# Kernel tuning notes

Hardware: AMD Instinct MI355X
Metric: run time of the kernel (lower is better)

The kernel has to match this reference:

```python
import jax, jax.numpy as jnp
import numpy as np
import math

N_LAYERS = 2; D = 768; D_INNER = 1536; N = 16; DR = 48; K = 4
VOCAB = 32000; B = 2; L = 1024
EPS = 1e-5


def setup_inputs() -> dict:
    key = jax.random.key(0)
    k = jax.random.split(key, 10)
    x = jax.random.randint(k[0], (B, L), 0, VOCAB)
    embedding = jax.random.normal(k[1], (VOCAB, D), jnp.float32) * 0.02
    rms_w = jnp.ones((N_LAYERS, D), jnp.float32)
    in_proj_w = jax.random.normal(k[2], (N_LAYERS, 2 * D_INNER, D), jnp.float32) * 0.02
    conv_w = jax.random.normal(k[3], (N_LAYERS, D_INNER, K), jnp.float32) * 0.1
    conv_b = jnp.zeros((N_LAYERS, D_INNER), jnp.float32)
    # S4D-real init: A[d, n] = n+1, stored as log(-A) = log(A)
    A0 = jnp.log(jnp.broadcast_to(jnp.arange(1, N + 1, dtype=jnp.float32), (D_INNER, N)))
    log_minus_A = jnp.tile(A0[None], (N_LAYERS, 1, 1))
    bcdelta_w = jax.random.normal(k[4], (N_LAYERS, 2 * N + DR, D_INNER), jnp.float32) * 0.02
    s = DR ** -0.5  # delta_init='random', delta_scale=1.0
    dup_w = jax.random.uniform(k[5], (N_LAYERS, D_INNER, DR), jnp.float32, minval=-s, maxval=s)
    u = jax.random.uniform(k[6], (N_LAYERS, D_INNER), jnp.float32)
    samp = jnp.maximum(jnp.exp((math.log(0.1) - math.log(0.001)) * u + math.log(0.001)), 1e-4)
    dup_b = samp + jnp.log(-jnp.expm1(-samp))  # softplus-inverse
    D_param = jnp.ones((N_LAYERS, D_INNER), jnp.float32)
    out_proj_w = jax.random.normal(k[7], (N_LAYERS, D, D_INNER), jnp.float32) * (0.02 / math.sqrt(N_LAYERS))
    norm_f_w = jnp.ones((D,), jnp.float32)
    return dict(x=x, embedding=embedding, rms_w=rms_w, in_proj_w=in_proj_w,
                conv_w=conv_w, conv_b=conv_b, log_minus_A=log_minus_A,
                bcdelta_w=bcdelta_w, dup_w=dup_w, dup_b=dup_b,
                D_param=D_param, out_proj_w=out_proj_w, norm_f_w=norm_f_w)


def _rmsnorm(h, w):
    return h * jax.lax.rsqrt(jnp.mean(h * h, axis=-1, keepdims=True) + EPS) * w


def _causal_conv(h, w, b):
    # depthwise causal conv: torch Conv1d(pad=K-1)[..., :L]
    hp = jnp.pad(h, ((0, 0), (K - 1, 0), (0, 0)))  # (b, l+K-1, d)
    Lh = h.shape[1]
    y = sum(hp[:, k:k + Lh, :] * w[:, k] for k in range(K))
    return y + b


def _s6(h, lA, bcw, dw, db, Dp):
    bcd = h @ bcw.T                                    # (b, l, 2N+DR)
    Bm, Cm, dlt = jnp.split(bcd, [N, 2 * N], axis=-1)
    delta = jax.nn.softplus(dlt @ dw.T + db)           # (b, l, d)
    A = -jnp.exp(lA)                                   # (d, n), negative
    dA = jnp.einsum('bld,dn->bldn', delta, A)
    A_bar = jnp.exp(dA)
    B_bar = (A_bar - 1.0) / dA * jnp.einsum('bld,bln->bldn', delta, Bm)
    u = B_bar * h[..., None]                           # (b, l, d, n)

    def step(hs, inp):
        a, ui, c = inp
        hs = a * hs + ui                               # (b, d, n)
        return hs, jnp.einsum('bn,bdn->bd', c, hs)

    h0 = jnp.zeros((h.shape[0], h.shape[2], N), h.dtype)
    _, ys = jax.lax.scan(step, h0, (jnp.swapaxes(A_bar, 0, 1),
                                    jnp.swapaxes(u, 0, 1),
                                    jnp.swapaxes(Cm, 0, 1)))
    return jnp.swapaxes(ys, 0, 1) + h * Dp


def _block(h, in_w, cw, cb, lA, bcw, dw, db, Dp, ow):
    xz = h @ in_w.T
    xi, res = jnp.split(xz, 2, axis=-1)
    xi = jax.nn.silu(_causal_conv(xi, cw, cb))
    y = _s6(xi, lA, bcw, dw, db, Dp)
    return (y * jax.nn.silu(res)) @ ow.T


def reference(x, embedding, rms_w, in_proj_w, conv_w, conv_b, log_minus_A,
              bcdelta_w, dup_w, dup_b, D_param, out_proj_w, norm_f_w):
    h = embedding[x]                                   # (b, l, D)
    for i in range(N_LAYERS):
        h = _block(_rmsnorm(h, rms_w[i]), in_proj_w[i], conv_w[i], conv_b[i],
                   log_minus_A[i], bcdelta_w[i], dup_w[i], dup_b[i],
                   D_param[i], out_proj_w[i]) + h
    h = _rmsnorm(h, norm_f_w)
    return h @ embedding.T                             # tied logits (b, l, V)
```

## Files before the change

kernel.cpp:

```cpp
#include <hip/hip_runtime.h>
#include <math.h>

#define BB 2
#define LL 1024
#define DD 768
#define DI 1536
#define NS 16
#define DRR 48
#define KC 4
#define VOC 32000
#define BT (BB*LL)
#define EPS 1e-5f

#define NCH 16
#define TC  (LL/NCH)
#define CHW ((DI/16)*256)

typedef __attribute__((ext_vector_type(4))) float f32x4;
typedef __attribute__((ext_vector_type(8))) short short8;
typedef unsigned short ushort_t;

__device__ __forceinline__ unsigned short f2bf(float f) {
    unsigned int u = __float_as_uint(f);
    u += 0x7FFFu + ((u >> 16) & 1u);
    return (unsigned short)(u >> 16);
}

#define GLDS(gp, lp) __builtin_amdgcn_global_load_lds( \
    (const __attribute__((address_space(1))) unsigned int*)(gp), \
    (__attribute__((address_space(3))) unsigned int*)(lp), 16, 0, 0)

#define DPP_ADD(c, ctrl) ((c) + __int_as_float(__builtin_amdgcn_update_dpp( \
    0, __float_as_int(c), (ctrl), 0xF, 0xF, true)))

template<bool ADD, bool NMASK, bool ATOMIC>
__global__ __launch_bounds__(256) void gemm_bf16(
    const ushort_t* __restrict__ A, const ushort_t* __restrict__ W,
    float* C, int Nn, int lda, int ldc, int kchunk)
{
    __shared__ __align__(16) ushort_t As[128 * 32];
    __shared__ __align__(16) ushort_t Ws[128 * 32];

    const int row0 = blockIdx.x * 128;
    const int col0 = blockIdx.y * 128;
    const int tid  = threadIdx.x;
    const int lane = tid & 63;
    const int wave = tid >> 6;
    const int wm   = (wave & 1) * 64;
    const int wn   = (wave >> 1) * 64;
    const int mrow = lane & 15;
    const int quad = lane >> 4;

    const int kb = blockIdx.z * kchunk;

    const int srow = tid >> 2;
    const int scol = (tid & 3) << 3;
    const ushort_t* gA0 = A + (size_t)(row0 + srow) * lda + scol;
    const ushort_t* gA1 = A + (size_t)(row0 + 64 + srow) * lda + scol;
    const ushort_t* gW0 = W + (size_t)(col0 + srow) * lda + scol;
    const ushort_t* gW1 = W + (size_t)(col0 + 64 + srow) * lda + scol;
    char* lA0 = (char*)As + wave * 1024;
    char* lA1 = (char*)As + 4096 + wave * 1024;
    char* lW0 = (char*)Ws + wave * 1024;
    char* lW1 = (char*)Ws + 4096 + wave * 1024;

    f32x4 acc[4][4];
#pragma unroll
    for (int i = 0; i < 4; ++i)
#pragma unroll
        for (int j = 0; j < 4; ++j)
            acc[i][j] = (f32x4){0.f, 0.f, 0.f, 0.f};

    for (int k0 = kb; k0 < kb + kchunk; k0 += 32) {
        GLDS(gA0 + k0, lA0);
        GLDS(gA1 + k0, lA1);
        GLDS(gW0 + k0, lW0);
        GLDS(gW1 + k0, lW1);
        __syncthreads();

        short8 af[4], wf[4];
#pragma unroll
        for (int i = 0; i < 4; ++i) {
            af[i] = *(const short8*)&As[(wm + i * 16 + mrow) * 32 + quad * 8];
            wf[i] = *(const short8*)&Ws[(wn + i * 16 + mrow) * 32 + quad * 8];
        }
#pragma unroll
        for (int i = 0; i < 4; ++i)
#pragma unroll
            for (int j = 0; j < 4; ++j)
                acc[i][j] = __builtin_amdgcn_mfma_f32_16x16x32_bf16(
                    af[i], wf[j], acc[i][j], 0, 0, 0);
        __syncthreads();
    }

#pragma unroll
    for (int i = 0; i < 4; ++i)
#pragma unroll
        for (int j = 0; j < 4; ++j)
#pragma unroll
            for (int r = 0; r < 4; ++r) {
                int row = row0 + wm + i * 16 + quad * 4 + r;
                int col = col0 + wn + j * 16 + mrow;
                if (!NMASK || col < Nn) {
                    float v = acc[i][j][r];
                    size_t off = (size_t)row * ldc + col;
                    if (ATOMIC) {
                        atomicAdd(&C[off], v);
                    } else {
                        if (ADD) v += C[off];
                        C[off] = v;
                    }
                }
            }
}

#define GK  768
#define GN  32000
#define NT12 12

__device__ __forceinline__ void stage_unit(
    int j, char* ldsw, const char* sA0, const char* sA1,
    const char* sB0, const char* sB1)
{
    if (j >= 4 * NT12) return;
    int tt = j >> 2, hh = (j >> 1) & 1, ee = j & 1;
    int koff = tt * 128 + hh * 64;
    char* dst = ldsw + (j & 7) * 16384;
    const char* s0 = (ee ? sB0 : sA0) + koff;
    const char* s1 = (ee ? sB1 : sA1) + koff;
    GLDS(s0, dst);
    GLDS(s1, dst + 8192);
}

#define VMCNT(N) asm volatile("s_waitcnt vmcnt(" #N ")" ::: "memory")

#define SBAR() do { __builtin_amdgcn_sched_barrier(0); \
    __builtin_amdgcn_s_barrier(); \
    __builtin_amdgcn_sched_barrier(0); } while (0)

#define MFMA16(M2) do { \
    __builtin_amdgcn_s_setprio(1); \
    _Pragma("unroll") \
    for (int i_ = 0; i_ < 4; ++i_) \
        _Pragma("unroll") \
        for (int n_ = 0; n_ < 4; ++n_) \
            acc[(M2)*4 + i_][n_] = __builtin_amdgcn_mfma_f32_16x16x32_bf16( \
                af[i_], wf[n_], acc[(M2)*4 + i_][n_], 0, 0, 0); \
    __builtin_amdgcn_s_setprio(0); \
} while (0)

#define PHASE(T, H, M2, LOADB, WAITSTMT) do { \
    const char* bufA_ = ldsc + ((T) & 1) * 65536 + (H) * 32768; \
    if (LOADB) { \
        _Pragma("unroll") \
        for (int n_ = 0; n_ < 4; ++n_) \
            wf[n_] = *(const short8*)(bufA_ + 16384 + offB[n_]); \
    } \
    _Pragma("unroll") \
    for (int i_ = 0; i_ < 4; ++i_) \
        af[i_] = *(const short8*)(bufA_ + offA[(M2)*4 + i_]); \
    stage_unit(4*(T) + 2*(H) + (M2) + 6, ldsw, sA0, sA1, sB0, sB1); \
    SBAR(); \
    MFMA16(M2); \
    WAITSTMT; \
    SBAR(); \
} while (0)

#define TILE(T, W1, W2) do { \
    PHASE(T, 0, 0, true,  (void)0); \
    PHASE(T, 0, 1, false, W1); \
    PHASE(T, 1, 0, true,  (void)0); \
    PHASE(T, 1, 1, false, W2); \
} while (0)

__global__ __launch_bounds__(512, 2) void gemm_logits_256(
    const ushort_t* __restrict__ A, const ushort_t* __restrict__ W,
    float* __restrict__ C)
{
    __shared__ __align__(16) char ldsc[131072];

    const int bid = blockIdx.x;
    const int s   = (bid & 7) * 125 + (bid >> 3);
    const int mt  = s & 7;
    const int nt  = s >> 3;

    const int tid  = threadIdx.x;
    const int lane = tid & 63;
    const int wave = tid >> 6;
    const int wm   = wave >> 2;
    const int wn   = wave & 3;
    const int mrow = lane & 15;
    const int quad = lane >> 4;

    int offA[8], offB[4];
#pragma unroll
    for (int m = 0; m < 8; ++m) {
        int r = wm * 128 + m * 16 + mrow;
        offA[m] = r * 64 + ((quad * 16) ^ (((r >> 1) & 3) << 4));
    }
#pragma unroll
    for (int n = 0; n < 4; ++n) {
        int r = wn * 64 + n * 16 + mrow;
        offB[n] = r * 64 + ((quad * 16) ^ (((r >> 1) & 3) << 4));
    }

    const int X0 = tid * 16;
    const int L0 = X0 ^ (((X0 >> 7) & 3) << 4);
    const int r0 = L0 >> 6, c0 = L0 & 63;
    const char* sA0 = (const char*)A + ((size_t)(mt * 256 +       r0) * GK) * 2 + c0;
    const char* sA1 = (const char*)A + ((size_t)(mt * 256 + 128 + r0) * GK) * 2 + c0;
    const char* sB0 = (const char*)W + ((size_t)(nt * 256 +       r0) * GK) * 2 + c0;
    const char* sB1 = (const char*)W + ((size_t)(nt * 256 + 128 + r0) * GK) * 2 + c0;
    char* ldsw = ldsc + wave * 1024;

    f32x4 acc[8][4];
#pragma unroll
    for (int m = 0; m < 8; ++m)
#pragma unroll
        for (int n = 0; n < 4; ++n)
            acc[m][n] = (f32x4){0.f, 0.f, 0.f, 0.f};

    short8 af[4], wf[4];

#pragma unroll
    for (int j = 0; j < 6; ++j)
        stage_unit(j, ldsw, sA0, sA1, sB0, sB1);
    VMCNT(8);
    SBAR();

    for (int t = 0; t < NT12 - 2; ++t)
        TILE(t, VMCNT(8), VMCNT(8));
    TILE(10, VMCNT(8), VMCNT(4));
    TILE(11, VMCNT(0), (void)0);

    float* Cb = C + (size_t)(mt * 256 + wm * 128 + quad * 4) * GN
                  + nt * 256 + wn * 64 + mrow;
#pragma unroll
    for (int m = 0; m < 8; ++m)
#pragma unroll
        for (int r = 0; r < 4; ++r)
#pragma unroll
            for (int n = 0; n < 4; ++n)
                Cb[(size_t)(m * 16 + r) * GN + n * 16] = acc[m][n][r];
}

__global__ __launch_bounds__(256) void cvt_bf16_kernel(
    const float* __restrict__ in, ushort_t* __restrict__ out, int n4)
{
    int i = blockIdx.x * 256 + threadIdx.x;
    if (i >= n4) return;
    float4 v = ((const float4*)in)[i];
    ushort4 o;
    o.x = f2bf(v.x); o.y = f2bf(v.y); o.z = f2bf(v.z); o.w = f2bf(v.w);
    ((ushort4*)out)[i] = o;
}

__global__ __launch_bounds__(256) void cvt_bcw_kernel(
    const float* __restrict__ bcw, ushort_t* __restrict__ out)
{
    int i = blockIdx.x * 256 + threadIdx.x;
    if (i >= 2 * 128 * 1536 / 4) return;
    int e = i * 4;
    int layer = e / (128 * 1536);
    int rem = e % (128 * 1536);
    int row = rem / 1536, col = rem % 1536;
    ushort4 o = {0, 0, 0, 0};
    if (row < 80) {
        float4 v = *(const float4*)(bcw + ((size_t)layer * 80 + row) * 1536 + col);
        o.x = f2bf(v.x); o.y = f2bf(v.y); o.z = f2bf(v.z); o.w = f2bf(v.w);
    }
    ((ushort4*)out)[i] = o;
}

__global__ __launch_bounds__(256) void zero_kernel(float* __restrict__ p, int n)
{
    int i = blockIdx.x * 256 + threadIdx.x;
    if (i < n) p[i] = 0.f;
}

__global__ __launch_bounds__(256) void embed_kernel(
    const int* __restrict__ x, const float* __restrict__ emb, float* __restrict__ h)
{
    int idx = blockIdx.x * 256 + threadIdx.x;
    if (idx >= BT * (DD / 4)) return;
    int row = idx / (DD / 4), c = idx % (DD / 4);
    ((float4*)h)[idx] = ((const float4*)(emb + (size_t)x[row] * DD))[c];
}

__global__ __launch_bounds__(256) void rmsnorm_kernel(
    const float* __restrict__ h, const float* __restrict__ w, ushort_t* __restrict__ out)
{
    int row = blockIdx.x, tid = threadIdx.x;
    const float* hr = h + (size_t)row * DD;
    float s = 0.f;
    for (int i = tid; i < DD; i += 256) { float v = hr[i]; s += v * v; }
#pragma unroll
    for (int off = 32; off >= 1; off >>= 1) s += __shfl_xor(s, off);
    __shared__ float part[4];
    if ((tid & 63) == 0) part[tid >> 6] = s;
    __syncthreads();
    float tot = part[0] + part[1] + part[2] + part[3];
    float sc = rsqrtf(tot * (1.0f / DD) + EPS);
    for (int i = tid; i < DD; i += 256)
        out[(size_t)row * DD + i] = f2bf(hr[i] * sc * w[i]);
}

__global__ __launch_bounds__(256) void conv_silu_kernel(
    const float* __restrict__ xz, const float* __restrict__ cw,
    const float* __restrict__ cb, float* __restrict__ xi, ushort_t* __restrict__ xi16)
{
    int idx = blockIdx.x * 256 + threadIdx.x;
    if (idx >= BT * DI) return;
    int d = idx % DI, bt = idx / DI, t = bt % LL;
    const float* base = xz + (size_t)bt * (2 * DI) + d;
    float w0 = cw[d * 4 + 0], w1 = cw[d * 4 + 1], w2 = cw[d * 4 + 2], w3 = cw[d * 4 + 3];
    float acc = cb[d] + base[0] * w3;
    if (t >= 1) acc += base[-(ptrdiff_t)(2 * DI)] * w2;
    if (t >= 2) acc += base[-(ptrdiff_t)(4 * DI)] * w1;
    if (t >= 3) acc += base[-(ptrdiff_t)(6 * DI)] * w0;
    float v = acc / (1.0f + expf(-acc));
    xi[idx] = v;
    xi16[idx] = f2bf(v);
}

__global__ __launch_bounds__(256) void delta_kernel(
    const float* __restrict__ bcd, const float* __restrict__ dw,
    const float* __restrict__ db, float* __restrict__ delta)
{
    int row = blockIdx.x / 6, chunk = blockIdx.x % 6;
    int d = chunk * 256 + threadIdx.x;
    __shared__ float dlt_s[DRR];
    if (threadIdx.x < DRR) dlt_s[threadIdx.x] = bcd[(size_t)row * 80 + 32 + threadIdx.x];
    __syncthreads();
    float z = db[d];
    const float* wr = dw + (size_t)d * DRR;
#pragma unroll
    for (int r = 0; r < DRR; ++r) z = fmaf(dlt_s[r], wr[r], z);
    delta[(size_t)row * DI + d] = (z > 20.f) ? z : log1pf(expf(z));
}

__global__ __launch_bounds__(256) void scan_pass1(
    const float* __restrict__ delta, const float* __restrict__ xi,
    const float* __restrict__ bcd, const float* __restrict__ lA,
    float* __restrict__ a_cum, float* __restrict__ h_end)
{
    int blk  = blockIdx.x;
    int c    = blk % NCH;
    int rest = blk / NCH;
    int b    = rest / (DI / 16);
    int dbi  = rest % (DI / 16);
    int dblk = dbi * 16;
    int tid  = threadIdx.x, lane = tid & 63, wave = tid >> 6;
    int n = lane & 15, dl = wave * 4 + (lane >> 4), d = dblk + dl;

    float Av   = -expf(lA[(size_t)d * NS + n]);
    float A2   = Av * 1.44269504088896f;
    float invA = 1.0f / Av;

    __shared__ float2 s_dx[TC][16];
    __shared__ float  s_B [TC][16];

    const float* dbase = delta + ((size_t)b * LL + c * TC) * DI + dblk;
    const float* xbase = xi    + ((size_t)b * LL + c * TC) * DI + dblk;
    const float* bcb   = bcd   + ((size_t)b * LL + c * TC) * 80;

    for (int i = tid; i < TC * 16; i += 256) {
        int tt = i >> 4, dd = i & 15;
        s_dx[tt][dd] = make_float2(dbase[(size_t)tt * DI + dd],
                                   xbase[(size_t)tt * DI + dd]);
        s_B[tt][dd]  = bcb[(size_t)tt * 80 + dd];
    }
    __syncthreads();

    float hs = 0.f, sd = 0.f;
#pragma unroll 4
    for (int tt = 0; tt < TC; ++tt) {
        float2 dx = s_dx[tt][dl];
        float Bv  = s_B[tt][n];
        float Ab  = exp2f(dx.x * A2);
        float u   = (Ab - 1.0f) * invA * Bv * dx.y;
        hs = fmaf(Ab, hs, u);
        sd += dx.x;
    }
    size_t o = (((size_t)b * NCH + c) * (DI / 16) + dbi) * 256 + dl * 16 + n;
    a_cum[o] = exp2f(A2 * sd);
    h_end[o] = hs;
}

__global__ __launch_bounds__(256) void scan_pass2(
    const float* __restrict__ a_cum, const float* __restrict__ h_end,
    float* __restrict__ h_init)
{
    int gid = blockIdx.x * 256 + threadIdx.x;
    if (gid >= BB * CHW) return;
    int b = gid / CHW, r = gid % CHW;
    size_t base = (size_t)b * NCH * CHW + r;
    float h = 0.f;
#pragma unroll
    for (int c = 0; c < NCH; ++c) {
        h_init[base + (size_t)c * CHW] = h;
        h = fmaf(a_cum[base + (size_t)c * CHW], h, h_end[base + (size_t)c * CHW]);
    }
}

__global__ __launch_bounds__(256) void scan_pass3(
    const float* __restrict__ delta, const float* __restrict__ xi,
    const float* __restrict__ bcd, const float* __restrict__ lA,
    const float* __restrict__ Dp, const float* __restrict__ h_init,
    float* __restrict__ y)
{
    int blk  = blockIdx.x;
    int c    = blk % NCH;
    int rest = blk / NCH;
    int b    = rest / (DI / 16);
    int dbi  = rest % (DI / 16);
    int dblk = dbi * 16;
    int tid  = threadIdx.x, lane = tid & 63, wave = tid >> 6;
    int n = lane & 15, dl = wave * 4 + (lane >> 4), d = dblk + dl;

    float Av   = -expf(lA[(size_t)d * NS + n]);
    float A2   = Av * 1.44269504088896f;
    float invA = 1.0f / Av;
    float Dpv  = Dp[d];

    __shared__ float2 s_dx[TC][16];
    __shared__ float2 s_bc[TC][16];

    const float* dbase = delta + ((size_t)b * LL + c * TC) * DI + dblk;
    const float* xbase = xi    + ((size_t)b * LL + c * TC) * DI + dblk;
    const float* bcb   = bcd   + ((size_t)b * LL + c * TC) * 80;
    float*       ybase = y     + ((size_t)b * LL + c * TC) * DI + dblk;

    for (int i = tid; i < TC * 16; i += 256) {
        int tt = i >> 4, dd = i & 15;
        s_dx[tt][dd] = make_float2(dbase[(size_t)tt * DI + dd],
                                   xbase[(size_t)tt * DI + dd]);
        s_bc[tt][dd] = make_float2(bcb[(size_t)tt * 80 + dd],
                                   bcb[(size_t)tt * 80 + 16 + dd]);
    }
    __syncthreads();

    float hs = h_init[(((size_t)b * NCH + c) * (DI / 16) + dbi) * 256 + dl * 16 + n];

#pragma unroll 4
    for (int tt = 0; tt < TC; ++tt) {
        float2 dx = s_dx[tt][dl];
        float2 bc = s_bc[tt][n];
        float Ab  = exp2f(dx.x * A2);
        float u   = (Ab - 1.0f) * invA * bc.x * dx.y;
        hs = fmaf(Ab, hs, u);
        float r = bc.y * hs;
        r = DPP_ADD(r, 0xB1);
        r = DPP_ADD(r, 0x4E);
        r = DPP_ADD(r, 0x141);
        r = DPP_ADD(r, 0x140);
        if (n == 0) ybase[(size_t)tt * DI + dl] = fmaf(dx.y, Dpv, r);
    }
}

__global__ __launch_bounds__(256) void gate_kernel(
    const float* __restrict__ y, const float* __restrict__ xz, ushort_t* __restrict__ yg16)
{
    int idx = blockIdx.x * 256 + threadIdx.x;
    if (idx >= BT * DI) return;
    int d = idx % DI, bt = idx / DI;
    float r = xz[(size_t)bt * (2 * DI) + DI + d];
    yg16[idx] = f2bf(y[idx] * r / (1.0f + expf(-r)));
}

extern "C" void kernel_launch(void* const* d_in, const int* in_sizes, int n_in,
                              void* d_out, int out_size, void* d_ws, size_t ws_size,
                              hipStream_t stream)
{
    const int*   x    = (const int*)  d_in[0];
    const float* emb  = (const float*)d_in[1];
    const float* rmsw = (const float*)d_in[2];
    const float* inw  = (const float*)d_in[3];
    const float* cw   = (const float*)d_in[4];
    const float* cb   = (const float*)d_in[5];
    const float* lA   = (const float*)d_in[6];
    const float* bcw  = (const float*)d_in[7];
    const float* dw   = (const float*)d_in[8];
    const float* db   = (const float*)d_in[9];
    const float* Dp   = (const float*)d_in[10];
    const float* ow   = (const float*)d_in[11];
    const float* nfw  = (const float*)d_in[12];
    float* out = (float*)d_out;

    float* ws = (float*)d_ws;
    float* h    = ws;
    float* xz   = h    + (size_t)BT * DD;
    float* xi   = xz   + (size_t)BT * 2 * DI;
    float* bcd  = xi   + (size_t)BT * DI;
    float* dlt  = bcd  + (size_t)BT * 80;
    float* yb   = dlt  + (size_t)BT * DI;
    float* acum = yb   + (size_t)BT * DI;
    float* hend = acum + (size_t)BB * NCH * DI * NS;
    float* hini = hend + (size_t)BB * NCH * DI * NS;
    ushort_t* bf = (ushort_t*)(hini + (size_t)BB * NCH * DI * NS);
    ushort_t* hn_bf  = bf;
    ushort_t* xib_bf = hn_bf  + (size_t)BT * DD;
    ushort_t* yg_bf  = xib_bf + (size_t)BT * DI;
    ushort_t* emb_bf = yg_bf  + (size_t)BT * DI;
    ushort_t* inw_bf = emb_bf + (size_t)VOC * DD;
    ushort_t* ow_bf  = inw_bf + (size_t)2 * 2 * DI * DD;
    ushort_t* bcw_bf = ow_bf  + (size_t)2 * DD * DI;

    cvt_bf16_kernel<<<(VOC * DD / 4 + 255) / 256, 256, 0, stream>>>(emb, emb_bf, VOC * DD / 4);
    cvt_bf16_kernel<<<(2 * 2 * DI * DD / 4 + 255) / 256, 256, 0, stream>>>(inw, inw_bf, 2 * 2 * DI * DD / 4);
    cvt_bf16_kernel<<<(2 * DD * DI / 4 + 255) / 256, 256, 0, stream>>>(ow, ow_bf, 2 * DD * DI / 4);
    cvt_bcw_kernel<<<(2 * 128 * 1536 / 4 + 255) / 256, 256, 0, stream>>>(bcw, bcw_bf);

    embed_kernel<<<(BT * (DD / 4) + 255) / 256, 256, 0, stream>>>(x, emb, h);

    for (int layer = 0; layer < 2; ++layer) {
        rmsnorm_kernel<<<BT, 256, 0, stream>>>(h, rmsw + (size_t)layer * DD, hn_bf);

        gemm_bf16<false, false, false><<<dim3(BT / 128, 2 * DI / 128, 1), 256, 0, stream>>>(
            hn_bf, inw_bf + (size_t)layer * 2 * DI * DD, xz, 2 * DI, DD, 2 * DI, DD);

        conv_silu_kernel<<<(BT * DI + 255) / 256, 256, 0, stream>>>(
            xz, cw + (size_t)layer * DI * KC, cb + (size_t)layer * DI, xi, xib_bf);

        zero_kernel<<<(BT * 80 + 255) / 256, 256, 0, stream>>>(bcd, BT * 80);

        gemm_bf16<false, true, true><<<dim3(BT / 128, 1, 8), 256, 0, stream>>>(
            xib_bf, bcw_bf + (size_t)layer * 128 * 1536, bcd, 80, DI, 80, DI / 8);

        delta_kernel<<<BT * 6, 256, 0, stream>>>(
            bcd, dw + (size_t)layer * DI * DRR, db + (size_t)layer * DI, dlt);

        scan_pass1<<<BB * (DI / 16) * NCH, 256, 0, stream>>>(
            dlt, xi, bcd, lA + (size_t)layer * DI * NS, acum, hend);
        scan_pass2<<<(BB * CHW + 255) / 256, 256, 0, stream>>>(acum, hend, hini);
        scan_pass3<<<BB * (DI / 16) * NCH, 256, 0, stream>>>(
            dlt, xi, bcd, lA + (size_t)layer * DI * NS, Dp + (size_t)layer * DI, hini, yb);

        gate_kernel<<<(BT * DI + 255) / 256, 256, 0, stream>>>(yb, xz, yg_bf);

        gemm_bf16<true, false, false><<<dim3(BT / 128, DD / 128, 1), 256, 0, stream>>>(
            yg_bf, ow_bf + (size_t)layer * DD * DI, h, DD, DI, DD, DI);
    }

    rmsnorm_kernel<<<BT, 256, 0, stream>>>(h, nfw, hn_bf);

    gemm_logits_256<<<dim3(BT / 256 * (VOC / 256)), 512, 0, stream>>>(
        hn_bf, emb_bf, out);
}
```

Measured before the change: 880.4 us.

## Double-buffer GEMM LDS, fuse embed+norm, gate into scan, split-K out_proj

Makes the bf16 GEMM double-buffered in LDS so the next K-tile's global loads are issued while MFMAs run on the current tile. It fuses the embedding gather with the first RMSNorm, folds the bcd zeroing into the conv kernel, and moves the SiLU gate into scan_pass3 so the fp32 y buffer and the separate gate kernel go away. The out_proj GEMM becomes split-K by 4 with atomic adds into h, and the logits stores become nontemporal. These changes cut launches and intermediate memory traffic, at the cost of double the GEMM LDS use, atomic contention, and nondeterministic summation order.

```diff
diff --git a/kernel.cpp b/kernel.cpp
--- a/kernel.cpp
+++ b/kernel.cpp
@@ -38,8 +38,8 @@
     const ushort_t* __restrict__ A, const ushort_t* __restrict__ W,
     float* C, int Nn, int lda, int ldc, int kchunk)
 {
-    __shared__ __align__(16) ushort_t As[128 * 32];
-    __shared__ __align__(16) ushort_t Ws[128 * 32];
+    __shared__ __align__(16) ushort_t As[2 * 128 * 32];
+    __shared__ __align__(16) ushort_t Ws[2 * 128 * 32];
 
     const int row0 = blockIdx.x * 128;
     const int col0 = blockIdx.y * 128;
@@ -50,8 +50,7 @@
     const int wn   = (wave >> 1) * 64;
     const int mrow = lane & 15;
     const int quad = lane >> 4;
-
-    const int kb = blockIdx.z * kchunk;
+    const int kb   = blockIdx.z * kchunk;
 
     const int srow = tid >> 2;
     const int scol = (tid & 3) << 3;
@@ -59,10 +58,13 @@
     const ushort_t* gA1 = A + (size_t)(row0 + 64 + srow) * lda + scol;
     const ushort_t* gW0 = W + (size_t)(col0 + srow) * lda + scol;
     const ushort_t* gW1 = W + (size_t)(col0 + 64 + srow) * lda + scol;
-    char* lA0 = (char*)As + wave * 1024;
-    char* lA1 = (char*)As + 4096 + wave * 1024;
-    char* lW0 = (char*)Ws + wave * 1024;
-    char* lW1 = (char*)Ws + 4096 + wave * 1024;
+
+#define STAGE_MM(buf, kk) do { \
+    char* a_ = (char*)As + (buf) * 8192 + wave * 1024; \
+    char* w_ = (char*)Ws + (buf) * 8192 + wave * 1024; \
+    GLDS(gA0 + (kk), a_); GLDS(gA1 + (kk), a_ + 4096); \
+    GLDS(gW0 + (kk), w_); GLDS(gW1 + (kk), w_ + 4096); \
+} while (0)
 
     f32x4 acc[4][4];
 #pragma unroll
@@ -71,18 +73,20 @@
         for (int j = 0; j < 4; ++j)
             acc[i][j] = (f32x4){0.f, 0.f, 0.f, 0.f};
 
+    STAGE_MM(0, kb);
+    __syncthreads();
+
+    int cur = 0;
     for (int k0 = kb; k0 < kb + kchunk; k0 += 32) {
-        GLDS(gA0 + k0, lA0);
-        GLDS(gA1 + k0, lA1);
-        GLDS(gW0 + k0, lW0);
-        GLDS(gW1 + k0, lW1);
-        __syncthreads();
-
+        if (k0 + 32 < kb + kchunk) STAGE_MM(cur ^ 1, k0 + 32);
+
+        const ushort_t* Ab = As + cur * 4096;
+        const ushort_t* Wb = Ws + cur * 4096;
         short8 af[4], wf[4];
 #pragma unroll
         for (int i = 0; i < 4; ++i) {
-            af[i] = *(const short8*)&As[(wm + i * 16 + mrow) * 32 + quad * 8];
-            wf[i] = *(const short8*)&Ws[(wn + i * 16 + mrow) * 32 + quad * 8];
+            af[i] = *(const short8*)&Ab[(wm + i * 16 + mrow) * 32 + quad * 8];
+            wf[i] = *(const short8*)&Wb[(wn + i * 16 + mrow) * 32 + quad * 8];
         }
 #pragma unroll
         for (int i = 0; i < 4; ++i)
@@ -91,7 +95,9 @@
                 acc[i][j] = __builtin_amdgcn_mfma_f32_16x16x32_bf16(
                     af[i], wf[j], acc[i][j], 0, 0, 0);
         __syncthreads();
-    }
+        cur ^= 1;
+    }
+#undef STAGE_MM
 
 #pragma unroll
     for (int i = 0; i < 4; ++i)
@@ -241,7 +247,8 @@
         for (int r = 0; r < 4; ++r)
 #pragma unroll
             for (int n = 0; n < 4; ++n)
-                Cb[(size_t)(m * 16 + r) * GN + n * 16] = acc[m][n][r];
+                __builtin_nontemporal_store(acc[m][n][r],
+                    &Cb[(size_t)(m * 16 + r) * GN + n * 16]);
 }
 
 __global__ __launch_bounds__(256) void cvt_bf16_kernel(
@@ -272,19 +279,26 @@
     ((ushort4*)out)[i] = o;
 }
 
-__global__ __launch_bounds__(256) void zero_kernel(float* __restrict__ p, int n)
-{
-    int i = blockIdx.x * 256 + threadIdx.x;
-    if (i < n) p[i] = 0.f;
-}
-
-__global__ __launch_bounds__(256) void embed_kernel(
-    const int* __restrict__ x, const float* __restrict__ emb, float* __restrict__ h)
-{
-    int idx = blockIdx.x * 256 + threadIdx.x;
-    if (idx >= BT * (DD / 4)) return;
-    int row = idx / (DD / 4), c = idx % (DD / 4);
-    ((float4*)h)[idx] = ((const float4*)(emb + (size_t)x[row] * DD))[c];
+__global__ __launch_bounds__(256) void embed_norm_kernel(
+    const int* __restrict__ x, const float* __restrict__ emb,
+    const float* __restrict__ w, float* __restrict__ h, ushort_t* __restrict__ out)
+{
+    int row = blockIdx.x, tid = threadIdx.x;
+    const float* er = emb + (size_t)x[row] * DD;
+    float v0 = er[tid], v1 = er[tid + 256], v2 = er[tid + 512];
+    float s = v0 * v0 + v1 * v1 + v2 * v2;
+#pragma unroll
+    for (int off = 32; off >= 1; off >>= 1) s += __shfl_xor(s, off);
+    __shared__ float part[4];
+    if ((tid & 63) == 0) part[tid >> 6] = s;
+    __syncthreads();
+    float sc = rsqrtf((part[0] + part[1] + part[2] + part[3]) * (1.0f / DD) + EPS);
+    float* hr = h + (size_t)row * DD;
+    hr[tid] = v0; hr[tid + 256] = v1; hr[tid + 512] = v2;
+    ushort_t* o = out + (size_t)row * DD;
+    o[tid]       = f2bf(v0 * sc * w[tid]);
+    o[tid + 256] = f2bf(v1 * sc * w[tid + 256]);
+    o[tid + 512] = f2bf(v2 * sc * w[tid + 512]);
 }
 
 __global__ __launch_bounds__(256) void rmsnorm_kernel(
@@ -307,10 +321,12 @@
 
 __global__ __launch_bounds__(256) void conv_silu_kernel(
     const float* __restrict__ xz, const float* __restrict__ cw,
-    const float* __restrict__ cb, float* __restrict__ xi, ushort_t* __restrict__ xi16)
+    const float* __restrict__ cb, float* __restrict__ xi, ushort_t* __restrict__ xi16,
+    float* __restrict__ bcd)
 {
     int idx = blockIdx.x * 256 + threadIdx.x;
     if (idx >= BT * DI) return;
+    if (idx < BT * 80) bcd[idx] = 0.f;
     int d = idx % DI, bt = idx / DI, t = bt % LL;
     const float* base = xz + (size_t)bt * (2 * DI) + d;
     float w0 = cw[d * 4 + 0], w1 = cw[d * 4 + 1], w2 = cw[d * 4 + 2], w3 = cw[d * 4 + 3];
@@ -407,7 +423,7 @@
     const float* __restrict__ delta, const float* __restrict__ xi,
     const float* __restrict__ bcd, const float* __restrict__ lA,
     const float* __restrict__ Dp, const float* __restrict__ h_init,
-    float* __restrict__ y)
+    const float* __restrict__ xz, ushort_t* __restrict__ yg)
 {
     int blk  = blockIdx.x;
     int c    = blk % NCH;
@@ -425,11 +441,13 @@
 
     __shared__ float2 s_dx[TC][16];
     __shared__ float2 s_bc[TC][16];
+    __shared__ float  s_rs[TC][16];
 
     const float* dbase = delta + ((size_t)b * LL + c * TC) * DI + dblk;
     const float* xbase = xi    + ((size_t)b * LL + c * TC) * DI + dblk;
     const float* bcb   = bcd   + ((size_t)b * LL + c * TC) * 80;
-    float*       ybase = y     + ((size_t)b * LL + c * TC) * DI + dblk;
+    const float* rbase = xz    + ((size_t)b * LL + c * TC) * (2 * DI) + DI + dblk;
+    ushort_t*    ygb   = yg    + ((size_t)b * LL + c * TC) * DI + dblk;
 
     for (int i = tid; i < TC * 16; i += 256) {
         int tt = i >> 4, dd = i & 15;
@@ -437,6 +455,7 @@
                                    xbase[(size_t)tt * DI + dd]);
         s_bc[tt][dd] = make_float2(bcb[(size_t)tt * 80 + dd],
                                    bcb[(size_t)tt * 80 + 16 + dd]);
+        s_rs[tt][dd] = rbase[(size_t)tt * (2 * DI) + dd];
     }
     __syncthreads();
 
@@ -454,18 +473,12 @@
         r = DPP_ADD(r, 0x4E);
         r = DPP_ADD(r, 0x141);
         r = DPP_ADD(r, 0x140);
-        if (n == 0) ybase[(size_t)tt * DI + dl] = fmaf(dx.y, Dpv, r);
-    }
-}
-
-__global__ __launch_bounds__(256) void gate_kernel(
-    const float* __restrict__ y, const float* __restrict__ xz, ushort_t* __restrict__ yg16)
-{
-    int idx = blockIdx.x * 256 + threadIdx.x;
-    if (idx >= BT * DI) return;
-    int d = idx % DI, bt = idx / DI;
-    float r = xz[(size_t)bt * (2 * DI) + DI + d];
-    yg16[idx] = f2bf(y[idx] * r / (1.0f + expf(-r)));
+        if (n == 0) {
+            float res = s_rs[tt][dl];
+            float yv  = fmaf(dx.y, Dpv, r);
+            ygb[(size_t)tt * DI + dl] = f2bf(yv * res / (1.0f + expf(-res)));
+        }
+    }
 }
 
 extern "C" void kernel_launch(void* const* d_in, const int* in_sizes, int n_in,
@@ -493,8 +506,7 @@
     float* xi   = xz   + (size_t)BT * 2 * DI;
     float* bcd  = xi   + (size_t)BT * DI;
     float* dlt  = bcd  + (size_t)BT * 80;
-    float* yb   = dlt  + (size_t)BT * DI;
-    float* acum = yb   + (size_t)BT * DI;
+    float* acum = dlt  + (size_t)BT * DI;
     float* hend = acum + (size_t)BB * NCH * DI * NS;
     float* hini = hend + (size_t)BB * NCH * DI * NS;
     ushort_t* bf = (ushort_t*)(hini + (size_t)BB * NCH * DI * NS);
@@ -511,18 +523,17 @@
     cvt_bf16_kernel<<<(2 * DD * DI / 4 + 255) / 256, 256, 0, stream>>>(ow, ow_bf, 2 * DD * DI / 4);
     cvt_bcw_kernel<<<(2 * 128 * 1536 / 4 + 255) / 256, 256, 0, stream>>>(bcw, bcw_bf);
 
-    embed_kernel<<<(BT * (DD / 4) + 255) / 256, 256, 0, stream>>>(x, emb, h);
+    embed_norm_kernel<<<BT, 256, 0, stream>>>(x, emb, rmsw, h, hn_bf);
 
     for (int layer = 0; layer < 2; ++layer) {
-        rmsnorm_kernel<<<BT, 256, 0, stream>>>(h, rmsw + (size_t)layer * DD, hn_bf);
+        if (layer)
+            rmsnorm_kernel<<<BT, 256, 0, stream>>>(h, rmsw + (size_t)layer * DD, hn_bf);
 
         gemm_bf16<false, false, false><<<dim3(BT / 128, 2 * DI / 128, 1), 256, 0, stream>>>(
             hn_bf, inw_bf + (size_t)layer * 2 * DI * DD, xz, 2 * DI, DD, 2 * DI, DD);
 
         conv_silu_kernel<<<(BT * DI + 255) / 256, 256, 0, stream>>>(
-            xz, cw + (size_t)layer * DI * KC, cb + (size_t)layer * DI, xi, xib_bf);
-
-        zero_kernel<<<(BT * 80 + 255) / 256, 256, 0, stream>>>(bcd, BT * 80);
+            xz, cw + (size_t)layer * DI * KC, cb + (size_t)layer * DI, xi, xib_bf, bcd);
 
         gemm_bf16<false, true, true><<<dim3(BT / 128, 1, 8), 256, 0, stream>>>(
             xib_bf, bcw_bf + (size_t)layer * 128 * 1536, bcd, 80, DI, 80, DI / 8);
@@ -534,12 +545,11 @@
             dlt, xi, bcd, lA + (size_t)layer * DI * NS, acum, hend);
         scan_pass2<<<(BB * CHW + 255) / 256, 256, 0, stream>>>(acum, hend, hini);
         scan_pass3<<<BB * (DI / 16) * NCH, 256, 0, stream>>>(
-            dlt, xi, bcd, lA + (size_t)layer * DI * NS, Dp + (size_t)layer * DI, hini, yb);
-
-        gate_kernel<<<(BT * DI + 255) / 256, 256, 0, stream>>>(yb, xz, yg_bf);
-
-        gemm_bf16<true, false, false><<<dim3(BT / 128, DD / 128, 1), 256, 0, stream>>>(
-            yg_bf, ow_bf + (size_t)layer * DD * DI, h, DD, DI, DD, DI);
+            dlt, xi, bcd, lA + (size_t)layer * DI * NS, Dp + (size_t)layer * DI, hini,
+            xz, yg_bf);
+
+        gemm_bf16<false, false, true><<<dim3(BT / 128, DD / 128, 4), 256, 0, stream>>>(
+            yg_bf, ow_bf + (size_t)layer * DD * DI, h, DD, DI, DD, DI / 4);
     }
 
     rmsnorm_kernel<<<BT, 256, 0, stream>>>(h, nfw, hn_bf);
```

After: 870.2 us. Within noise of the previous version (-1.2%).
